# Kernel optimization log

Hardware: AMD Instinct MI355X
Metric: run time of the kernel (lower is better)

## Reference

```python
import jax, jax.numpy as jnp
import numpy as np

N = 100000   # nodes
E = 1600000  # edges (avg degree 16)
IN = 128     # in_channels
H = 64       # num_hidden -> conv1 out = 2*H = 128
RRELU_SLOPE = (1.0 / 8.0 + 1.0 / 3.0) / 2.0  # F.rrelu eval: mean of (lower, upper)


def setup_inputs() -> dict:
    key = jax.random.key(0)
    k1, k2, k3, k4 = jax.random.split(key, 4)
    x = jax.random.normal(k1, (N, IN), dtype=jnp.float32)
    edge_index = jax.random.randint(k2, (2, E), 0, N, dtype=jnp.int32)
    # Glorot-ish init for the two GCN linear layers (PyG GCNConv has weight + bias)
    W1 = jax.random.normal(k3, (IN, 2 * H), dtype=jnp.float32) * (1.0 / np.sqrt(IN))
    b1 = jnp.zeros((2 * H,), dtype=jnp.float32)
    W2 = jax.random.normal(k4, (2 * H, H), dtype=jnp.float32) * (1.0 / np.sqrt(2 * H))
    b2 = jnp.zeros((H,), dtype=jnp.float32)
    return {"x": x, "edge_index": edge_index, "W1": W1, "b1": b1, "W2": W2, "b2": b2}


def _gcn_conv(x, row, col, norm, W, b, n):
    # PyG GCNConv: transform, gather source nodes, scale by sym norm, scatter-add to targets
    h = x @ W                                   # [N, out]
    msg = h[row] * norm[:, None]                # [E+N, out] gathered messages
    return jax.ops.segment_sum(msg, col, num_segments=n) + b


def reference(x, edge_index, W1, b1, W2, b2):
    n = x.shape[0]
    loops = jnp.arange(n, dtype=edge_index.dtype)
    row = jnp.concatenate([edge_index[0], loops])  # sources (with self-loops)
    col = jnp.concatenate([edge_index[1], loops])  # targets (with self-loops)
    deg = jax.ops.segment_sum(jnp.ones_like(col, dtype=x.dtype), col, num_segments=n)
    dinv = jnp.where(deg > 0, jax.lax.rsqrt(deg), 0.0)
    norm = dinv[row] * dinv[col]                  # deg^{-1/2}[u] * deg^{-1/2}[v]
    h = _gcn_conv(x, row, col, norm, W1, b1, n)
    h = jnp.where(h >= 0, h, RRELU_SLOPE * h)     # rrelu (eval mode)
    return _gcn_conv(h, row, col, norm, W2, b2, n)
```

## Files before the change

### kernel.cpp

```cpp
#include <hip/hip_runtime.h>


#define C_IN   128
#define C_MID  128
#define C_OUT2 64
#define SLOT_CAP 64
#define SORT_SH  9
#define SORT_W   196
#define SORT_CAP 16384
#define P1_EPT   32

typedef __attribute__((ext_vector_type(8))) short short8;
typedef __attribute__((ext_vector_type(4))) float floatx4;
typedef __attribute__((ext_vector_type(2))) float f32x2;

__device__ __constant__ float kSlope = 0.22916666666666666f;

__device__ __forceinline__ unsigned short f2bf(float f) {
    unsigned u = __builtin_bit_cast(unsigned, f);
    u = (u + 0x7fffu + ((u >> 16) & 1u)) >> 16;
    return (unsigned short)u;
}
__device__ __forceinline__ f32x2 bfpair(int x) {
    return (f32x2){__builtin_bit_cast(float, (unsigned)x << 16),
                   __builtin_bit_cast(float, (unsigned)(x & 0xffff0000))};
}

__global__ __launch_bounds__(256) void sort_prep_kernel(
        const int* __restrict__ ei, int2* __restrict__ sorted,
        int* __restrict__ bcur,
        const float* __restrict__ W1, const float* __restrict__ W2,
        ushort* __restrict__ W1T, ushort* __restrict__ W2T,
        int E, int p1b) {
    if (blockIdx.x >= p1b) {
        int t = (blockIdx.x - p1b) * 256 + threadIdx.x;
        if (t < C_MID * C_IN) {
            int nn = t >> 7, k = t & 127;
            W1T[t] = f2bf(W1[k * C_MID + nn]);
        } else {
            int i = t - C_MID * C_IN;
            if (i < C_OUT2 * C_MID) {
                int nn = i >> 7, k = i & 127;
                W2T[i] = f2bf(W2[k * C_OUT2 + nn]);
            }
        }
        return;
    }
    __shared__ int hist[SORT_W], goff[SORT_W], cur[SORT_W];
    const int tid = threadIdx.x;
    for (int i = tid; i < SORT_W; i += 256) { hist[i] = 0; cur[i] = 0; }
    __syncthreads();
    const int base = blockIdx.x * (P1_EPT * 256);
#pragma unroll 4
    for (int k = 0; k < P1_EPT; ++k) {
        int e = base + k * 256 + tid;
        if (e < E) atomicAdd(&hist[ei[E + e] >> SORT_SH], 1);
    }
    __syncthreads();
    for (int i = tid; i < SORT_W; i += 256)
        if (hist[i]) goff[i] = atomicAdd(&bcur[i], hist[i]);
    __syncthreads();
#pragma unroll 4
    for (int k = 0; k < P1_EPT; ++k) {
        int e = base + k * 256 + tid;
        if (e < E) {
            int v = ei[E + e], u = ei[e];
            int b = v >> SORT_SH;
            int p = goff[b] + atomicAdd(&cur[b], 1);
            if (p < SORT_CAP) sorted[(size_t)b * SORT_CAP + p] = (int2){u, v};
        }
    }
}

template <int CO, bool ABF>
__device__ __forceinline__ void gemm_body(char* smem, int row0,
        const void* __restrict__ Xv, const ushort* __restrict__ WT,
        ushort* __restrict__ Y, int n) {
    constexpr int LDW = 136;
    constexpr int NT = CO / 16;
    ushort* Ws = (ushort*)smem;
    const int tid = threadIdx.x, wave = tid >> 6, lane = tid & 63;
    const int m = lane & 15, q = lane >> 4;

#pragma unroll
    for (int c = 0; c < CO / 16; ++c) {
        int id = tid + c * 256;
        int r = id >> 4, h8 = id & 15;
        *(int4*)&Ws[r * LDW + h8 * 8] = ((const int4*)(WT + r * C_IN))[h8];
    }
    __syncthreads();

    const int rowA = min(row0 + wave * 16 + m, n - 1);
    floatx4 acc[NT];
#pragma unroll
    for (int c = 0; c < NT; ++c) acc[c] = (floatx4){0.f, 0.f, 0.f, 0.f};

#pragma unroll
    for (int s = 0; s < 4; ++s) {
        short8 af;
        if constexpr (ABF) {
            af = *(const short8*)((const ushort*)Xv + (size_t)rowA * C_IN + s * 32 + q * 8);
        } else {
            const float* xp = (const float*)Xv + (size_t)rowA * C_IN + s * 32 + q * 8;
            float4 a0 = *(const float4*)xp;
            float4 a1 = *(const float4*)(xp + 4);
            union { unsigned short us[8]; short8 v; } t;
            t.us[0] = f2bf(a0.x); t.us[1] = f2bf(a0.y); t.us[2] = f2bf(a0.z); t.us[3] = f2bf(a0.w);
            t.us[4] = f2bf(a1.x); t.us[5] = f2bf(a1.y); t.us[6] = f2bf(a1.z); t.us[7] = f2bf(a1.w);
            af = t.v;
        }
#pragma unroll
        for (int c = 0; c < NT; ++c) {
            short8 bf = *(short8*)&Ws[(c * 16 + m) * LDW + s * 32 + q * 8];
            acc[c] = __builtin_amdgcn_mfma_f32_16x16x32_bf16(af, bf, acc[c], 0, 0, 0);
        }
    }
#pragma unroll
    for (int c = 0; c < NT; ++c)
#pragma unroll
        for (int i = 0; i < 4; ++i) {
            int rr = row0 + wave * 16 + q * 4 + i;
            if (rr < n) Y[(size_t)rr * CO + c * 16 + m] = f2bf(acc[c][i]);
        }
}

__global__ __launch_bounds__(256) void csr_gemm1_kernel(
        const int2* __restrict__ sorted, const int* __restrict__ bcur,
        int* __restrict__ cnt, float* __restrict__ dinv,
        int* __restrict__ slots,
        const float* __restrict__ X, const ushort* __restrict__ W1T,
        ushort* __restrict__ h1, int n) {
    __shared__ __align__(16) char smem[C_MID * 136 * 2];
    if (blockIdx.x < SORT_W) {
        int* lc = (int*)smem;
        const int b = blockIdx.x, tid = threadIdx.x;
        const int base_v = b << SORT_SH;
        for (int i = tid; i < 512; i += 256) lc[i] = 0;
        __syncthreads();
        const int nb = min(bcur[b], SORT_CAP);
        const int2* src = sorted + (size_t)b * SORT_CAP;
        for (int i = tid; i < nb; i += 256) {
            int2 e = src[i];
            int pos = atomicAdd(&lc[e.y - base_v], 1);
            if (pos < SLOT_CAP - 1) slots[(size_t)e.y * SLOT_CAP + pos] = e.x;
        }
        __syncthreads();
        for (int i = tid; i < 512; i += 256) {
            int v = base_v + i;
            if (v < n) {
                int deg = lc[i];
                int st = min(deg, SLOT_CAP - 1);
                slots[(size_t)v * SLOT_CAP + st] = v;
                cnt[v] = st + 1;
                dinv[v] = rsqrtf((float)(deg + 1));
            }
        }
        return;
    }
    gemm_body<C_MID, false>(smem, (blockIdx.x - SORT_W) * 64, X, W1T, h1, n);
}

template <int CO, bool ABF>
__global__ __launch_bounds__(256) void gemm_mfma(const void* __restrict__ Xv,
                                                 const ushort* __restrict__ WT,
                                                 ushort* __restrict__ Y, int n) {
    __shared__ __align__(16) char smem[CO * 136 * 2];
    gemm_body<CO, ABF>(smem, blockIdx.x * 64, Xv, WT, Y, n);
}

template <int C, bool DO_RRELU, bool OUT_BF>
__global__ __launch_bounds__(256) void agg_kernel(const ushort* __restrict__ H,
                                                  const int* __restrict__ slots,
                                                  const int* __restrict__ cnt,
                                                  const float* __restrict__ dinv,
                                                  const float* __restrict__ bias,
                                                  void* __restrict__ outv, int n) {
    constexpr int GS = C / 8;
    constexpr int NG = 64 / GS;
    constexpr int NCH = 24 / NG;
    const int wave = threadIdx.x >> 6, lane = threadIdx.x & 63;
    const int v = blockIdx.x * 4 + wave;
    if (v >= n) return;

    const float dv = dinv[v];
    const int lim = cnt[v];
    const int last = lim - 1;
    const int* sl = slots + (size_t)v * SLOT_CAP;
    int u_l = (lane < lim) ? sl[lane] : v;
    float w_l = dinv[u_l] * dv;

    const int g = lane / GS, s = lane % GS;

    float ww[NCH];
    int4 dd[NCH];
#pragma unroll
    for (int t = 0; t < NCH; ++t) {
        int jj = t * NG + g;
        int c = jj < last ? jj : last;
        int u = __shfl(u_l, c);
        float wv = __shfl(w_l, c);
        ww[t] = (jj < lim) ? wv : 0.f;
        dd[t] = *(const int4*)(H + (size_t)u * C + s * 8);
    }
    f32x2 acc[4];
#pragma unroll
    for (int k = 0; k < 4; ++k) acc[k] = (f32x2){0.f, 0.f};
#pragma unroll
    for (int t = 0; t < NCH; ++t) {
        acc[0] += bfpair(dd[t].x) * ww[t];
        acc[1] += bfpair(dd[t].y) * ww[t];
        acc[2] += bfpair(dd[t].z) * ww[t];
        acc[3] += bfpair(dd[t].w) * ww[t];
    }
    for (int j = 24; j < lim; j += NG) {
        int jj = j + g;
        int c = jj < last ? jj : last;
        int u = __shfl(u_l, c);
        float wv = __shfl(w_l, c);
        float wgt = (jj < lim) ? wv : 0.f;
        const int4 d = *(const int4*)(H + (size_t)u * C + s * 8);
        acc[0] += bfpair(d.x) * wgt; acc[1] += bfpair(d.y) * wgt;
        acc[2] += bfpair(d.z) * wgt; acc[3] += bfpair(d.w) * wgt;
    }

    float a[8];
#pragma unroll
    for (int k = 0; k < 4; ++k) { a[2 * k] = acc[k].x; a[2 * k + 1] = acc[k].y; }
#pragma unroll
    for (int k = 0; k < 8; ++k)
#pragma unroll
        for (int off = GS; off < 64; off <<= 1)
            a[k] += __shfl_xor(a[k], off);

    if (g == 0) {
        float r[8];
#pragma unroll
        for (int k = 0; k < 8; ++k) {
            r[k] = a[k] + bias[s * 8 + k];
            if (DO_RRELU) r[k] = (r[k] >= 0.f) ? r[k] : r[k] * kSlope;
        }
        if constexpr (OUT_BF) {
            union { ushort us[8]; int4 v; } o;
#pragma unroll
            for (int k = 0; k < 8; ++k) o.us[k] = f2bf(r[k]);
            *(int4*)((ushort*)outv + (size_t)v * C + s * 8) = o.v;
        } else {
            float* op = (float*)outv + (size_t)v * C + s * 8;
            *(float4*)op       = (float4){r[0], r[1], r[2], r[3]};
            *(float4*)(op + 4) = (float4){r[4], r[5], r[6], r[7]};
        }
    }
}

extern "C" void kernel_launch(void* const* d_in, const int* in_sizes, int n_in,
                              void* d_out, int out_size, void* d_ws, size_t ws_size,
                              hipStream_t stream) {
    const float* x  = (const float*)d_in[0];
    const int*   ei = (const int*)d_in[1];
    const float* W1 = (const float*)d_in[2];
    const float* b1 = (const float*)d_in[3];
    const float* W2 = (const float*)d_in[4];
    const float* b2 = (const float*)d_in[5];
    const int n = in_sizes[0] / C_IN;
    const int E = in_sizes[1] / 2;

    char* w = (char*)d_ws;
    auto alloc = [&](size_t bytes) -> char* {
        char* p = w; w += (bytes + 255) & ~(size_t)255; return p;
    };
    int*    cnt    = (int*)alloc((size_t)n * 4);
    float*  dinv   = (float*)alloc((size_t)n * 4);
    int*    slots  = (int*)alloc((size_t)n * SLOT_CAP * 4);
    ushort* h1     = (ushort*)alloc((size_t)n * C_MID * 2);
    ushort* h2     = (ushort*)alloc((size_t)n * C_MID * 2);
    ushort* h3     = h1;
    ushort* W1T    = (ushort*)alloc((size_t)C_MID * C_IN * 2);
    ushort* W2T    = (ushort*)alloc((size_t)C_OUT2 * C_MID * 2);
    int2*   sorted = (int2*)alloc((size_t)SORT_W * SORT_CAP * 8);
    int*    bcur   = (int*)alloc((size_t)SORT_W * 4);

    const int p1b = (E + P1_EPT * 256 - 1) / (P1_EPT * 256);
    const int prep_blocks = (C_MID * C_IN + C_OUT2 * C_MID + 255) / 256;
    const int gemm1_blocks = (n + 63) / 64;

    hipMemsetAsync(bcur, 0, (size_t)SORT_W * 4, stream);
    sort_prep_kernel<<<p1b + prep_blocks, 256, 0, stream>>>(
        ei, sorted, bcur, W1, W2, W1T, W2T, E, p1b);
    csr_gemm1_kernel<<<SORT_W + gemm1_blocks, 256, 0, stream>>>(
        sorted, bcur, cnt, dinv, slots, x, W1T, h1, n);
    agg_kernel<C_MID, true, true><<<(n + 3) / 4, 256, 0, stream>>>(
        h1, slots, cnt, dinv, b1, h2, n);
    gemm_mfma<C_OUT2, true><<<(n + 63) / 64, 256, 0, stream>>>(h2, W2T, h3, n);
    agg_kernel<C_OUT2, false, false><<<(n + 3) / 4, 256, 0, stream>>>(
        h3, slots, cnt, dinv, b2, d_out, n);
}
```

Measured before the change: 273.8 us.

## Process two nodes per wave in aggregation and shrink sort edges-per-thread

The aggregation kernel now has each wavefront handle two destination nodes, interleaving their neighbor gathers so more independent loads are in flight, and launches half as many blocks. Neighbor indices are loaded unconditionally and clamped to valid range instead of being masked by count. Separately, the edge-bucketing kernel processes 8 edges per thread instead of 32 with full unrolling, producing more blocks. The cost is doubled register pressure in the aggregation kernel, which may lower occupancy, and more global bucket atomics in the sort.

```diff
diff --git a/kernel.cpp b/kernel.cpp
--- a/kernel.cpp
+++ b/kernel.cpp
@@ -8,7 +8,7 @@
 #define SORT_SH  9
 #define SORT_W   196
 #define SORT_CAP 16384
-#define P1_EPT   32
+#define P1_EPT   8
 
 typedef __attribute__((ext_vector_type(8))) short short8;
 typedef __attribute__((ext_vector_type(4))) float floatx4;
@@ -51,7 +51,7 @@
     for (int i = tid; i < SORT_W; i += 256) { hist[i] = 0; cur[i] = 0; }
     __syncthreads();
     const int base = blockIdx.x * (P1_EPT * 256);
-#pragma unroll 4
+#pragma unroll
     for (int k = 0; k < P1_EPT; ++k) {
         int e = base + k * 256 + tid;
         if (e < E) atomicAdd(&hist[ei[E + e] >> SORT_SH], 1);
@@ -60,7 +60,7 @@
     for (int i = tid; i < SORT_W; i += 256)
         if (hist[i]) goff[i] = atomicAdd(&bcur[i], hist[i]);
     __syncthreads();
-#pragma unroll 4
+#pragma unroll
     for (int k = 0; k < P1_EPT; ++k) {
         int e = base + k * 256 + tid;
         if (e < E) {
@@ -179,71 +179,95 @@
     constexpr int NG = 64 / GS;
     constexpr int NCH = 24 / NG;
     const int wave = threadIdx.x >> 6, lane = threadIdx.x & 63;
-    const int v = blockIdx.x * 4 + wave;
-    if (v >= n) return;
-
-    const float dv = dinv[v];
-    const int lim = cnt[v];
-    const int last = lim - 1;
-    const int* sl = slots + (size_t)v * SLOT_CAP;
-    int u_l = (lane < lim) ? sl[lane] : v;
-    float w_l = dinv[u_l] * dv;
+    const int vA = blockIdx.x * 8 + wave * 2;
+    if (vA >= n) return;
+    const int vB = (vA + 1 < n) ? vA + 1 : vA;
+
+    int rawA = slots[(size_t)vA * SLOT_CAP + lane];
+    int rawB = slots[(size_t)vB * SLOT_CAP + lane];
+    const int limA = cnt[vA], limB = cnt[vB];
+    const float dvA = dinv[vA], dvB = dinv[vB];
+    const int uA = min(max(rawA, 0), n - 1);
+    const int uB = min(max(rawB, 0), n - 1);
+    const float wA_l = dinv[uA] * dvA;
+    const float wB_l = dinv[uB] * dvB;
+    const int lastA = limA - 1, lastB = limB - 1;
 
     const int g = lane / GS, s = lane % GS;
 
-    float ww[NCH];
-    int4 dd[NCH];
+    float wwA[NCH], wwB[NCH];
+    int4 ddA[NCH], ddB[NCH];
 #pragma unroll
     for (int t = 0; t < NCH; ++t) {
         int jj = t * NG + g;
-        int c = jj < last ? jj : last;
-        int u = __shfl(u_l, c);
-        float wv = __shfl(w_l, c);
-        ww[t] = (jj < lim) ? wv : 0.f;
-        dd[t] = *(const int4*)(H + (size_t)u * C + s * 8);
-    }
-    f32x2 acc[4];
-#pragma unroll
-    for (int k = 0; k < 4; ++k) acc[k] = (f32x2){0.f, 0.f};
+        int cA = jj < lastA ? jj : lastA;
+        int cB = jj < lastB ? jj : lastB;
+        int usA = __shfl(uA, cA), usB = __shfl(uB, cB);
+        float wsA = __shfl(wA_l, cA), wsB = __shfl(wB_l, cB);
+        wwA[t] = (jj < limA) ? wsA : 0.f;
+        wwB[t] = (jj < limB) ? wsB : 0.f;
+        ddA[t] = *(const int4*)(H + (size_t)usA * C + s * 8);
+        ddB[t] = *(const int4*)(H + (size_t)usB * C + s * 8);
+    }
+    f32x2 accA[4], accB[4];
+#pragma unroll
+    for (int k = 0; k < 4; ++k) { accA[k] = (f32x2){0.f, 0.f}; accB[k] = (f32x2){0.f, 0.f}; }
 #pragma unroll
     for (int t = 0; t < NCH; ++t) {
-        acc[0] += bfpair(dd[t].x) * ww[t];
-        acc[1] += bfpair(dd[t].y) * ww[t];
-        acc[2] += bfpair(dd[t].z) * ww[t];
-        acc[3] += bfpair(dd[t].w) * ww[t];
-    }
-    for (int j = 24; j < lim; j += NG) {
+        accA[0] += bfpair(ddA[t].x) * wwA[t]; accA[1] += bfpair(ddA[t].y) * wwA[t];
+        accA[2] += bfpair(ddA[t].z) * wwA[t]; accA[3] += bfpair(ddA[t].w) * wwA[t];
+        accB[0] += bfpair(ddB[t].x) * wwB[t]; accB[1] += bfpair(ddB[t].y) * wwB[t];
+        accB[2] += bfpair(ddB[t].z) * wwB[t]; accB[3] += bfpair(ddB[t].w) * wwB[t];
+    }
+    for (int j = 24; j < limA; j += NG) {
         int jj = j + g;
-        int c = jj < last ? jj : last;
-        int u = __shfl(u_l, c);
-        float wv = __shfl(w_l, c);
-        float wgt = (jj < lim) ? wv : 0.f;
+        int c = jj < lastA ? jj : lastA;
+        int u = __shfl(uA, c);
+        float wv = __shfl(wA_l, c);
+        float wgt = (jj < limA) ? wv : 0.f;
         const int4 d = *(const int4*)(H + (size_t)u * C + s * 8);
-        acc[0] += bfpair(d.x) * wgt; acc[1] += bfpair(d.y) * wgt;
-        acc[2] += bfpair(d.z) * wgt; acc[3] += bfpair(d.w) * wgt;
-    }
-
-    float a[8];
-#pragma unroll
-    for (int k = 0; k < 4; ++k) { a[2 * k] = acc[k].x; a[2 * k + 1] = acc[k].y; }
+        accA[0] += bfpair(d.x) * wgt; accA[1] += bfpair(d.y) * wgt;
+        accA[2] += bfpair(d.z) * wgt; accA[3] += bfpair(d.w) * wgt;
+    }
+    for (int j = 24; j < limB; j += NG) {
+        int jj = j + g;
+        int c = jj < lastB ? jj : lastB;
+        int u = __shfl(uB, c);
+        float wv = __shfl(wB_l, c);
+        float wgt = (jj < limB) ? wv : 0.f;
+        const int4 d = *(const int4*)(H + (size_t)u * C + s * 8);
+        accB[0] += bfpair(d.x) * wgt; accB[1] += bfpair(d.y) * wgt;
+        accB[2] += bfpair(d.z) * wgt; accB[3] += bfpair(d.w) * wgt;
+    }
+
+    float a[8], b8[8];
+#pragma unroll
+    for (int k = 0; k < 4; ++k) {
+        a[2 * k] = accA[k].x; a[2 * k + 1] = accA[k].y;
+        b8[2 * k] = accB[k].x; b8[2 * k + 1] = accB[k].y;
+    }
 #pragma unroll
     for (int k = 0; k < 8; ++k)
 #pragma unroll
-        for (int off = GS; off < 64; off <<= 1)
+        for (int off = GS; off < 64; off <<= 1) {
             a[k] += __shfl_xor(a[k], off);
-
-    if (g == 0) {
+            b8[k] += __shfl_xor(b8[k], off);
+        }
+
+    if (g < 2) {
+        const int v = (g == 0) ? vA : vB;
         float r[8];
 #pragma unroll
         for (int k = 0; k < 8; ++k) {
-            r[k] = a[k] + bias[s * 8 + k];
+            float t = (g == 0) ? a[k] : b8[k];
+            r[k] = t + bias[s * 8 + k];
             if (DO_RRELU) r[k] = (r[k] >= 0.f) ? r[k] : r[k] * kSlope;
         }
         if constexpr (OUT_BF) {
-            union { ushort us[8]; int4 v; } o;
+            union { ushort us[8]; int4 v4; } o;
 #pragma unroll
             for (int k = 0; k < 8; ++k) o.us[k] = f2bf(r[k]);
-            *(int4*)((ushort*)outv + (size_t)v * C + s * 8) = o.v;
+            *(int4*)((ushort*)outv + (size_t)v * C + s * 8) = o.v4;
         } else {
             float* op = (float*)outv + (size_t)v * C + s * 8;
             *(float4*)op       = (float4){r[0], r[1], r[2], r[3]};
@@ -288,9 +312,9 @@
         ei, sorted, bcur, W1, W2, W1T, W2T, E, p1b);
     csr_gemm1_kernel<<<SORT_W + gemm1_blocks, 256, 0, stream>>>(
         sorted, bcur, cnt, dinv, slots, x, W1T, h1, n);
-    agg_kernel<C_MID, true, true><<<(n + 3) / 4, 256, 0, stream>>>(
+    agg_kernel<C_MID, true, true><<<(n + 7) / 8, 256, 0, stream>>>(
         h1, slots, cnt, dinv, b1, h2, n);
     gemm_mfma<C_OUT2, true><<<(n + 63) / 64, 256, 0, stream>>>(h2, W2T, h3, n);
-    agg_kernel<C_OUT2, false, false><<<(n + 3) / 4, 256, 0, stream>>>(
+    agg_kernel<C_OUT2, false, false><<<(n + 7) / 8, 256, 0, stream>>>(
         h3, slots, cnt, dinv, b2, d_out, n);
 }
```

After: 271.2 us. About the same (-0.9%).
